# Performance work log

Measured on AMD Instinct MI355X. Metric: run time of the kernel, lower is better.

## Reference

```python
import jax, jax.numpy as jnp
import numpy as np

N = 200000   # nodes
E = 4000000  # edges
D = 32       # hidden dim (forced equal to edge-embed dim 32)
G = 512      # graphs in batch
OUT = 64     # conv5 output dim
BN_EPS = 1e-5


def _bn(h, g, b):
    # BatchNorm1d, training mode (fresh model): biased batch stats over node dim
    mu = jnp.mean(h, axis=0)
    var = jnp.var(h, axis=0)
    return g * (h - mu) * jax.lax.rsqrt(var + BN_EPS) + b


def _gine(h, src, dst, e, W1, b1, g, be, W2, b2, final_relu):
    # GINEConv (eps=0): out = MLP(x + sum_j ReLU(x_j + edge_attr))
    msg = jax.nn.relu(h[src] + e)                              # [E, D]
    agg = jax.ops.segment_sum(msg, dst, num_segments=h.shape[0])
    z = h + agg
    z = jax.nn.relu(_bn(z @ W1 + b1, g, be)) @ W2 + b2
    return jax.nn.relu(z) if final_relu else z


def setup_inputs() -> dict:
    key = jax.random.key(0)
    ks = jax.random.split(key, 16)
    xav = lambda k, shp: jax.random.uniform(k, shp, jnp.float32, -1.0, 1.0) * np.sqrt(6.0 / (shp[-2] + shp[-1]))
    x = jax.random.normal(ks[0], (N, D), jnp.float32)
    edge_index = jax.random.randint(ks[1], (2, E), 0, N, dtype=jnp.int32)
    edge_type = jax.random.randint(ks[2], (E,), 0, 2, dtype=jnp.int32)
    batch = jnp.sort(jax.random.randint(ks[3], (N,), 0, G, dtype=jnp.int32))
    emb = xav(ks[4], (2, D))  # xavier-initialized edge-type embedding
    # convs 1-4: Linear(D,D), BN(D), ReLU, Linear(D,D), ReLU  -> stacked [4,...]
    W1s = xav(ks[5], (4, D, D)); b1s = jnp.zeros((4, D))
    g1s = jnp.ones((4, D)); be1s = jnp.zeros((4, D))
    W2s = xav(ks[6], (4, D, D)); b2s = jnp.zeros((4, D))
    # conv 5: Linear(D,D), BN(D), ReLU, Linear(D,OUT)  (no final ReLU)
    w15 = xav(ks[7], (D, D)); b15 = jnp.zeros((D,))
    g5 = jnp.ones((D,)); be5 = jnp.zeros((D,))
    w25 = xav(ks[8], (D, OUT)); b25 = jnp.zeros((OUT,))
    return dict(x=x, edge_index=edge_index, edge_type=edge_type, batch=batch,
                emb=emb, W1s=W1s, b1s=b1s, g1s=g1s, be1s=be1s, W2s=W2s, b2s=b2s,
                w15=w15, b15=b15, g5=g5, be5=be5, w25=w25, b25=b25)


def reference(x, edge_index, edge_type, batch, emb, W1s, b1s, g1s, be1s, W2s, b2s,
              w15, b15, g5, be5, w25, b25):
    src, dst = edge_index[0], edge_index[1]
    e = emb[edge_type]                                          # [E, D]
    h = x
    for i in range(4):
        h = _gine(h, src, dst, e, W1s[i], b1s[i], g1s[i], be1s[i], W2s[i], b2s[i], True)
    h = _gine(h, src, dst, e, w15, b15, g5, be5, w25, b25, False)  # [N, OUT]
    mx = jax.ops.segment_max(h, batch, num_segments=G)
    cnt = jax.ops.segment_sum(jnp.ones((h.shape[0], 1), h.dtype), batch, num_segments=G)
    mn = jax.ops.segment_sum(h, batch, num_segments=G) / jnp.maximum(cnt, 1.0)
    return jnp.concatenate([mx, mn], axis=1)                    # [G, 2*OUT]
```

## Files before the change

kernel.cpp:

```cpp
#include <hip/hip_runtime.h>

#define NBLKA 2048

__device__ __forceinline__ unsigned encf(float x) {
    unsigned u = __float_as_uint(x);
    return (u & 0x80000000u) ? ~u : (u | 0x80000000u);
}
__device__ __forceinline__ float decf(unsigned u) {
    u = (u & 0x80000000u) ? (u & 0x7FFFFFFFu) : ~u;
    return __uint_as_float(u);
}
__device__ __forceinline__ unsigned bf16rne(float f) {
    unsigned u = __float_as_uint(f);
    return (u + 0x7FFFu + ((u >> 16) & 1u)) >> 16;
}


__global__ __launch_bounds__(256) void passA_k(const int* __restrict__ dst, int E,
                                               int* __restrict__ cntMat, int bshift,
                                               int nblk, int nb2) {
    __shared__ int hist[512];
    hist[threadIdx.x] = 0; hist[threadIdx.x + 256] = 0;
    __syncthreads();
    int base = blockIdx.x * 4096;
#pragma unroll
    for (int r = 0; r < 16; r++) {
        int i = base + threadIdx.x + r * 256;
        if (i < E) atomicAdd(&hist[dst[i] >> bshift], 1);
    }
    __syncthreads();
    for (int bk = threadIdx.x; bk < nb2; bk += 256)
        cntMat[bk * nblk + blockIdx.x] = hist[bk];
}

__global__ void scanA_k(int* __restrict__ data, int total, int* __restrict__ chunkTot) {
    __shared__ int sd[256];
    int tid = threadIdx.x;
    int base = blockIdx.x * 2048 + tid * 8;
    int v[8]; int s = 0;
#pragma unroll
    for (int r = 0; r < 8; r++) {
        int idx = base + r;
        int x = (idx < total) ? data[idx] : 0;
        s += x; v[r] = s;
    }
    sd[tid] = s; __syncthreads();
    for (int off = 1; off < 256; off <<= 1) {
        int x = (tid >= off) ? sd[tid - off] : 0;
        __syncthreads();
        sd[tid] += x;
        __syncthreads();
    }
    int prev = (tid > 0) ? sd[tid - 1] : 0;
#pragma unroll
    for (int r = 0; r < 8; r++) {
        int idx = base + r;
        if (idx < total) data[idx] = v[r] + prev;
    }
    if (tid == 255) chunkTot[blockIdx.x] = sd[255];
}

__global__ void scanB_k(const int* __restrict__ chunkTot, int nchunk, int* __restrict__ chunkOff) {
    __shared__ int sd[256];
    int tid = threadIdx.x;
    int v = (tid < nchunk) ? chunkTot[tid] : 0;
    sd[tid] = v; __syncthreads();
    for (int off = 1; off < 256; off <<= 1) {
        int x = (tid >= off) ? sd[tid - off] : 0;
        __syncthreads();
        sd[tid] += x;
        __syncthreads();
    }
    if (tid < nchunk) chunkOff[tid] = sd[tid] - v;
}

__global__ void scanC2_k(int* __restrict__ data, int total, const int* __restrict__ chunkOff) {
    int off = chunkOff[blockIdx.x];
    int base = blockIdx.x * 2048 + threadIdx.x * 8;
#pragma unroll
    for (int r = 0; r < 8; r++) {
        int idx = base + r;
        if (idx < total) data[idx] += off;
    }
}

__global__ __launch_bounds__(256) void passB_k(const int* __restrict__ ei,
                                               const int* __restrict__ ety, int E,
                                               const int* __restrict__ cntScan,
                                               unsigned* __restrict__ binned,
                                               int bshift, int sBits, int nblk, int nb2) {
    __shared__ unsigned stage[4096];
    __shared__ unsigned short bkid[4096];
    __shared__ int hist[512], sd[256], cursor[512], rebase[512];
    int tid = threadIdx.x;
    int base = blockIdx.x * 4096;
    hist[tid] = 0; hist[tid + 256] = 0;
    __syncthreads();

    unsigned ent[16];
    int bk[16];
    int lowmask = (1 << bshift) - 1;
    int dshift = sBits + 1;
#pragma unroll
    for (int r = 0; r < 16; r++) {
        int i = base + tid + r * 256;
        if (i < E) {
            int s = ei[i];
            int d = ei[E + i];
            int t = ety[i];
            ent[r] = ((unsigned)(d & lowmask) << dshift) | ((unsigned)t << sBits) | (unsigned)s;
            bk[r] = d >> bshift;
            atomicAdd(&hist[bk[r]], 1);
        } else bk[r] = -1;
    }
    __syncthreads();

    int v0 = hist[2 * tid], v1 = hist[2 * tid + 1];
    int sum2 = v0 + v1;
    sd[tid] = sum2; __syncthreads();
    for (int off = 1; off < 256; off <<= 1) {
        int x = (tid >= off) ? sd[tid - off] : 0;
        __syncthreads();
        sd[tid] += x;
        __syncthreads();
    }
    int exclPair = sd[tid] - sum2;
    __syncthreads();
    cursor[2 * tid] = exclPair;
    cursor[2 * tid + 1] = exclPair + v0;
    int b0 = 2 * tid, b1 = 2 * tid + 1;
    rebase[b0] = (b0 < nb2 && v0 > 0) ? (cntScan[b0 * nblk + blockIdx.x] - v0) - exclPair : 0;
    rebase[b1] = (b1 < nb2 && v1 > 0) ? (cntScan[b1 * nblk + blockIdx.x] - v1) - (exclPair + v0) : 0;
    __syncthreads();

#pragma unroll
    for (int r = 0; r < 16; r++) {
        if (bk[r] >= 0) {
            int p = atomicAdd(&cursor[bk[r]], 1);
            stage[p] = ent[r];
            bkid[p] = (unsigned short)bk[r];
        }
    }
    __syncthreads();

    int cnt = E - base; if (cnt > 4096) cnt = 4096;
    for (int i = tid; i < cnt; i += 256)
        binned[rebase[bkid[i]] + i] = stage[i];
}

__global__ __launch_bounds__(256) void passC_k(const unsigned* __restrict__ binned,
                                               const int* __restrict__ cntScan,
                                               int nblk, int* __restrict__ rowptr,
                                               unsigned* __restrict__ sorted,
                                               int N, int E, int bshift, int sBits,
                                               int nb2) {
    __shared__ int hist[512], cursor[512], sd[256];
    int tid = threadIdx.x;
    int b = blockIdx.x;
    int s = (b == 0) ? 0 : cntScan[b * nblk - 1];
    int e = cntScan[(b + 1) * nblk - 1];
    int nodeBase = b << bshift;
    int dshift = sBits + 1;

    hist[tid] = 0; hist[tid + 256] = 0;
    __syncthreads();
    for (int i = s + tid; i < e; i += 256)
        atomicAdd(&hist[(int)(binned[i] >> dshift)], 1);
    __syncthreads();

    int v0 = hist[2 * tid], v1 = hist[2 * tid + 1];
    int sum2 = v0 + v1;
    sd[tid] = sum2; __syncthreads();
    for (int off = 1; off < 256; off <<= 1) {
        int x = (tid >= off) ? sd[tid - off] : 0;
        __syncthreads();
        sd[tid] += x;
        __syncthreads();
    }
    int exclPair = sd[tid] - sum2;
    __syncthreads();
    cursor[2 * tid] = exclPair;
    cursor[2 * tid + 1] = exclPair + v0;
    int n0 = nodeBase + 2 * tid, n1 = nodeBase + 2 * tid + 1;
    if (n0 < N) rowptr[n0] = s + exclPair;
    if (n1 < N) rowptr[n1] = s + exclPair + v0;
    __syncthreads();

    for (int i = s + tid; i < e; i += 256) {
        unsigned en = binned[i];
        int ln = (int)(en >> dshift);
        int p = atomicAdd(&cursor[ln], 1);
        sorted[s + p] = en;
    }
    if (b == nb2 - 1 && tid == 0) rowptr[N] = E;
}

__global__ void prep_k(const float* __restrict__ x, unsigned* __restrict__ P,
                       unsigned* __restrict__ Q, int N,
                       unsigned* __restrict__ maxb, float* __restrict__ sumb, int G64) {
    int i = blockIdx.x * 256 + threadIdx.x;
    int tot = N * 16;
    if (i < tot) {
        float2 v = ((const float2*)x)[i];
        P[i] = bf16rne(v.x) | (bf16rne(v.y) << 16);
    }
    if (i < 16) {
        unsigned sp = bf16rne(-1e30f) | (bf16rne(-1e30f) << 16);
        P[tot + i] = sp;
        Q[tot + i] = sp;
    }
    if (i < G64) { maxb[i] = 0x007FFFFFu; sumb[i] = 0.f; }
}

__global__ __launch_bounds__(256) void layerA_k(
    const unsigned* __restrict__ hin, const int* __restrict__ rowptr,
    const unsigned* __restrict__ sorted, const float* __restrict__ emb,
    const float* __restrict__ W1, const float* __restrict__ b1,
    float* __restrict__ tout, float* __restrict__ partial, int Nn, int sBits,
    unsigned sentw)
{
    float2* tout2 = (float2*)tout;
    int tid = threadIdx.x;
    int gl = tid & 31;
    int c = gl & 15;
    int slot = gl >> 4;
    int grp = tid >> 5;
    unsigned smask = (1u << sBits) - 1u;

    float2 w1c[16];
#pragma unroll
    for (int kk = 0; kk < 16; kk++)
        w1c[kk] = *(const float2*)&W1[(16 * slot + kk) * 32 + 2 * c];
    float2 b1p = *(const float2*)&b1[2 * c];
    float2 e0p = *(const float2*)&emb[2 * c];
    float2 e1p = *(const float2*)&emb[32 + 2 * c];

    __shared__ float zl[8][32];
    __shared__ float ls[8][32], lq[8][32];

    float2 bsum = {0.f, 0.f}, bsq = {0.f, 0.f};

    int gid0 = (blockIdx.x * 256 + tid) >> 5;
    int nG = (gridDim.x * 256) >> 5;

    for (int n = gid0; n < Nn; n += nG) {
        int es = rowptr[n], ee = rowptr[n + 1];
        float accx = 0.f, accy = 0.f;
        for (int e0 = es; e0 < ee; e0 += 32) {
            int idx = e0 + gl;
            unsigned pv = (idx < ee) ? sorted[idx] : sentw;
#pragma unroll
            for (int kk = 0; kk < 16; kk++) {
                unsigned p = (unsigned)__shfl((int)pv, kk, 16);
                unsigned s = p & smask;
                unsigned w = hin[s * 16u + (unsigned)c];
                float hx = __uint_as_float(w << 16);
                float hy = __uint_as_float(w & 0xFFFF0000u);
                bool t1 = ((p >> sBits) & 1u) != 0u;
                float evx = t1 ? e1p.x : e0p.x;
                float evy = t1 ? e1p.y : e0p.y;
                accx += fmaxf(hx + evx, 0.f);
                accy += fmaxf(hy + evy, 0.f);
            }
        }
        accx += __shfl_xor(accx, 16);
        accy += __shfl_xor(accy, 16);
        unsigned wn = hin[(unsigned)n * 16u + (unsigned)c];
        accx += __uint_as_float(wn << 16);
        accy += __uint_as_float(wn & 0xFFFF0000u);

        if (slot == 0) { zl[grp][2 * c] = accx; zl[grp][2 * c + 1] = accy; }
        float tx = 0.f, ty = 0.f;
#pragma unroll
        for (int kk = 0; kk < 16; kk++) {
            float zk = zl[grp][16 * slot + kk];
            tx = fmaf(zk, w1c[kk].x, tx);
            ty = fmaf(zk, w1c[kk].y, ty);
        }
        tx += __shfl_xor(tx, 16);
        ty += __shfl_xor(ty, 16);
        tx += b1p.x; ty += b1p.y;
        if (slot == 0) { float2 tp; tp.x = tx; tp.y = ty; tout2[(unsigned)n * 16u + (unsigned)c] = tp; }
        bsum.x += tx; bsum.y += ty;
        bsq.x = fmaf(tx, tx, bsq.x);
        bsq.y = fmaf(ty, ty, bsq.y);
    }

    if (slot == 0) {
        ls[grp][2 * c] = bsum.x; ls[grp][2 * c + 1] = bsum.y;
        lq[grp][2 * c] = bsq.x;  lq[grp][2 * c + 1] = bsq.y;
    }
    __syncthreads();
    if (tid < 32) {
        float s = 0.f, q = 0.f;
#pragma unroll
        for (int r = 0; r < 8; r++) { s += ls[r][tid]; q += lq[r][tid]; }
        partial[blockIdx.x * 64 + tid] = s;
        partial[blockIdx.x * 64 + 32 + tid] = q;
    }
}

__global__ __launch_bounds__(256) void bnred1_k(const float* __restrict__ partial,
                                                float* __restrict__ partial2) {
    __shared__ float sd[4][64];
    int tid = threadIdx.x;
    int c = tid & 63, q = tid >> 6;
    int rowBase = blockIdx.x * 32 + q * 8;
    float s = 0.f;
#pragma unroll
    for (int r = 0; r < 8; r++) s += partial[(rowBase + r) * 64 + c];
    sd[q][c] = s;
    __syncthreads();
    if (q == 0) partial2[blockIdx.x * 64 + c] = sd[0][c] + sd[1][c] + sd[2][c] + sd[3][c];
}

__global__ __launch_bounds__(256) void bnred2_k(const float* __restrict__ partial2,
                                                const float* __restrict__ gamma,
                                                const float* __restrict__ beta,
                                                float* __restrict__ bn_ac, float invN) {
    __shared__ float sd[4][64];
    int tid = threadIdx.x;
    int c = tid & 63, q = tid >> 6;
    float s = 0.f;
#pragma unroll
    for (int r = 0; r < 16; r++) s += partial2[(q * 16 + r) * 64 + c];
    sd[q][c] = s;
    __syncthreads();
    if (tid < 32) {
        float mu  = (sd[0][tid] + sd[1][tid] + sd[2][tid] + sd[3][tid]) * invN;
        float sq  = (sd[0][tid + 32] + sd[1][tid + 32] + sd[2][tid + 32] + sd[3][tid + 32]) * invN;
        float var = sq - mu * mu;
        float a = gamma[tid] * rsqrtf(var + 1e-5f);
        bn_ac[tid] = a;
        bn_ac[32 + tid] = beta[tid] - a * mu;
    }
}

__global__ __launch_bounds__(256) void layerB32_k(
    const float* __restrict__ tin, const float* __restrict__ bn_ac,
    const float* __restrict__ W2, const float* __restrict__ b2,
    unsigned* __restrict__ hout, int Nn)
{
    int tid = threadIdx.x;
    int j = tid & 31, grp = tid >> 5;
    float a = bn_ac[j], c = bn_ac[32 + j];
    float wc[32];
#pragma unroll
    for (int k = 0; k < 32; k++) wc[k] = W2[k * 32 + j];
    float bj = b2[j];
    for (int n = blockIdx.x * 8 + grp; n < Nn; n += gridDim.x * 8) {
        float t = tin[n * 32 + j];
        float u = fmaxf(fmaf(a, t, c), 0.f);
        float o = bj;
#pragma unroll
        for (int k = 0; k < 32; k++) o = fmaf(__shfl(u, k, 32), wc[k], o);
        unsigned b = bf16rne(fmaxf(o, 0.f));
        unsigned nb = (unsigned)__shfl_xor((int)b, 1, 32);
        if ((j & 1) == 0) hout[(unsigned)n * 16u + (unsigned)(j >> 1)] = b | (nb << 16);
    }
}

__global__ __launch_bounds__(256) void layerB64pool_k(
    const float* __restrict__ tin, const float* __restrict__ bn_ac,
    const float* __restrict__ W2, const float* __restrict__ b2,
    const int* __restrict__ batch,
    unsigned* __restrict__ maxb, float* __restrict__ sumb, int Nn)
{
    int tid = threadIdx.x;
    int j = tid & 31, grp = tid >> 5;
    float a = bn_ac[j], c = bn_ac[32 + j];
    float wlo[32], whi[32];
#pragma unroll
    for (int k = 0; k < 32; k++) { wlo[k] = W2[k * 64 + j]; whi[k] = W2[k * 64 + 32 + j]; }
    float blo = b2[j], bhi = b2[32 + j];

    int n0 = (blockIdx.x * 8 + grp) * 64;
    if (n0 >= Nn) return;
    int nend = n0 + 64; if (nend > Nn) nend = Nn;

    int curg = -1;
    float mxl = 0.f, mxh = 0.f, sml = 0.f, smh = 0.f;
    for (int n = n0; n < nend; n++) {
        float t = tin[n * 32 + j];
        float u = fmaxf(fmaf(a, t, c), 0.f);
        float olo = blo, ohi = bhi;
#pragma unroll
        for (int k = 0; k < 32; k++) {
            float uk = __shfl(u, k, 32);
            olo = fmaf(uk, wlo[k], olo);
            ohi = fmaf(uk, whi[k], ohi);
        }
        int gn = batch[n];
        if (gn != curg) {
            if (curg >= 0) {
                atomicMax(&maxb[curg * 64 + j], encf(mxl));
                atomicMax(&maxb[curg * 64 + 32 + j], encf(mxh));
                atomicAdd(&sumb[curg * 64 + j], sml);
                atomicAdd(&sumb[curg * 64 + 32 + j], smh);
            }
            curg = gn; mxl = olo; mxh = ohi; sml = olo; smh = ohi;
        } else {
            mxl = fmaxf(mxl, olo); mxh = fmaxf(mxh, ohi);
            sml += olo; smh += ohi;
        }
    }
    if (curg >= 0) {
        atomicMax(&maxb[curg * 64 + j], encf(mxl));
        atomicMax(&maxb[curg * 64 + 32 + j], encf(mxh));
        atomicAdd(&sumb[curg * 64 + j], sml);
        atomicAdd(&sumb[curg * 64 + 32 + j], smh);
    }
}

__global__ void final_k(const unsigned* __restrict__ maxb, const float* __restrict__ sumb,
                        const int* __restrict__ batch, int Nn, float* __restrict__ out)
{
    int g = blockIdx.x, tid = threadIdx.x;
    int a = 0, b = Nn;
    while (a < b) { int m = (a + b) >> 1; if (batch[m] < g) a = m + 1; else b = m; }
    int lo0 = a;
    a = 0; b = Nn;
    while (a < b) { int m = (a + b) >> 1; if (batch[m] < g + 1) a = m + 1; else b = m; }
    int hi0 = a;
    float inv = 1.f / fmaxf((float)(hi0 - lo0), 1.f);
    if (tid < 64) out[g * 128 + tid] = decf(maxb[g * 64 + tid]);
    else          out[g * 128 + tid] = sumb[g * 64 + (tid - 64)] * inv;
}

extern "C" void kernel_launch(void* const* d_in, const int* in_sizes, int n_in,
                              void* d_out, int out_size, void* d_ws, size_t ws_size,
                              hipStream_t stream) {
    const float* x    = (const float*)d_in[0];
    const int*   ei   = (const int*)d_in[1];
    const int*   ety  = (const int*)d_in[2];
    const int*   batch= (const int*)d_in[3];
    const float* emb  = (const float*)d_in[4];
    const float* W1s  = (const float*)d_in[5];
    const float* b1s  = (const float*)d_in[6];
    const float* g1s  = (const float*)d_in[7];
    const float* be1s = (const float*)d_in[8];
    const float* W2s  = (const float*)d_in[9];
    const float* b2s  = (const float*)d_in[10];
    const float* w15  = (const float*)d_in[11];
    const float* b15  = (const float*)d_in[12];
    const float* g5   = (const float*)d_in[13];
    const float* be5  = (const float*)d_in[14];
    const float* w25  = (const float*)d_in[15];
    const float* b25  = (const float*)d_in[16];

    int N = in_sizes[0] / 32;
    int E = in_sizes[1] / 2;
    int G = out_size / 128;

    int sBits = 1; while ((1 << sBits) < N + 1) sBits++;
    int bshift = 0; while (((N - 1) >> bshift) >= 512) bshift++;
    int nb2 = ((N - 1) >> bshift) + 1;
    int nblkE = (E + 4095) / 4096;

    char* wsb = (char*)d_ws;
    size_t o = 0;
    size_t hPkBytes = (size_t)(N + 1) * 16 * 4;
    size_t tbBytes = (size_t)N * 32 * 4;
    size_t binBytes = (size_t)E * 4;
    size_t rtb = tbBytes > binBytes ? tbBytes : binBytes;
    unsigned* P      = (unsigned*)(wsb + o); o += hPkBytes;
    unsigned* Q      = (unsigned*)(wsb + o); o += hPkBytes;
    float*    tb     = (float*)(wsb + o);
    unsigned* binned = (unsigned*)(wsb + o);
    o += rtb;
    int*      rowptr = (int*)(wsb + o);   o += ((size_t)N + 2) * 4;
    unsigned* sorted = (unsigned*)(wsb + o); o += (size_t)E * 4;
    int*      chunkTot = (int*)(wsb + o); o += 1024;
    int*      chunkOff = (int*)(wsb + o); o += 1024;
    float*    partial  = (float*)(wsb + o); o += (size_t)NBLKA * 64 * 4;
    float*    partial2 = (float*)(wsb + o); o += 64 * 64 * 4;
    float*    bn_ac    = (float*)(wsb + o); o += 64 * 4;
    unsigned* maxb     = (unsigned*)(wsb + o); o += (size_t)G * 64 * 4;
    float*    sumb     = (float*)(wsb + o); o += (size_t)G * 64 * 4;
    int*      cntMat   = (int*)(wsb + o); o += (size_t)nb2 * nblkE * 4;

    passA_k<<<nblkE, 256, 0, stream>>>(ei + E, E, cntMat, bshift, nblkE, nb2);
    int total2 = nb2 * nblkE;
    int nchunk2 = (total2 + 2047) / 2048;
    scanA_k<<<nchunk2, 256, 0, stream>>>(cntMat, total2, chunkTot);
    scanB_k<<<1, 256, 0, stream>>>(chunkTot, nchunk2, chunkOff);
    scanC2_k<<<nchunk2, 256, 0, stream>>>(cntMat, total2, chunkOff);
    passB_k<<<nblkE, 256, 0, stream>>>(ei, ety, E, cntMat, binned, bshift, sBits, nblkE, nb2);
    passC_k<<<nb2, 256, 0, stream>>>(binned, cntMat, nblkE, rowptr, sorted, N, E, bshift, sBits, nb2);
    prep_k<<<(N * 16 + 255) / 256, 256, 0, stream>>>(x, P, Q, N, maxb, sumb, G * 64);

    unsigned sentw = (unsigned)N;
    float invN = 1.f / (float)N;

    unsigned* inb = P;
    unsigned* outb = Q;
    for (int L = 0; L < 5; ++L) {
        const float* W1 = (L < 4) ? W1s + L * 1024 : w15;
        const float* b1 = (L < 4) ? b1s + L * 32  : b15;
        const float* ga = (L < 4) ? g1s + L * 32  : g5;
        const float* be = (L < 4) ? be1s + L * 32 : be5;
        const float* W2 = (L < 4) ? W2s + L * 1024 : w25;
        const float* b2 = (L < 4) ? b2s + L * 32  : b25;

        layerA_k<<<NBLKA, 256, 0, stream>>>(inb, rowptr, sorted, emb, W1, b1, tb, partial, N, sBits, sentw);
        bnred1_k<<<64, 256, 0, stream>>>(partial, partial2);
        bnred2_k<<<1, 256, 0, stream>>>(partial2, ga, be, bn_ac, invN);
        if (L < 4) {
            layerB32_k<<<1024, 256, 0, stream>>>(tb, bn_ac, W2, b2, outb, N);
            unsigned* tmp = inb; inb = outb; outb = tmp;
        } else {
            layerB64pool_k<<<(N + 511) / 512, 256, 0, stream>>>(tb, bn_ac, W2, b2, batch, maxb, sumb, N);
        }
    }

    final_k<<<G, 128, 0, stream>>>(maxb, sumb, batch, N, (float*)d_out);
}
```

Measured before the change: 688.6 us.

## Switch node features to fp16 packed math and fuse small BN/scan kernels

Node features are now stored as packed fp16 instead of bf16, and the edge message add and ReLU use packed half2 arithmetic before accumulating in fp32. The goal is fewer ALU instructions per gathered edge in the hot aggregation loop. Separately, the single-block BN finalize kernel is folded into the prologue of each layerB block, and the scan offset kernel is merged into the add pass, removing five-plus small launches. The cost is that every layerB block redundantly recomputes the BN statistics, and fp16 has less range than bf16, so large activations could overflow.

```diff
diff --git a/kernel.cpp b/kernel.cpp
--- a/kernel.cpp
+++ b/kernel.cpp
@@ -1,6 +1,9 @@
 #include <hip/hip_runtime.h>
+#include <hip/hip_fp16.h>
 
 #define NBLKA 2048
+
+typedef _Float16 f16x2 __attribute__((ext_vector_type(2)));
 
 __device__ __forceinline__ unsigned encf(float x) {
     unsigned u = __float_as_uint(x);
@@ -9,10 +12,6 @@
 __device__ __forceinline__ float decf(unsigned u) {
     u = (u & 0x80000000u) ? (u & 0x7FFFFFFFu) : ~u;
     return __uint_as_float(u);
-}
-__device__ __forceinline__ unsigned bf16rne(float f) {
-    unsigned u = __float_as_uint(f);
-    return (u + 0x7FFFu + ((u >> 16) & 1u)) >> 16;
 }
 
 
@@ -60,7 +59,8 @@
     if (tid == 255) chunkTot[blockIdx.x] = sd[255];
 }
 
-__global__ void scanB_k(const int* __restrict__ chunkTot, int nchunk, int* __restrict__ chunkOff) {
+__global__ void scanC3_k(int* __restrict__ data, int total,
+                         const int* __restrict__ chunkTot, int nchunk) {
     __shared__ int sd[256];
     int tid = threadIdx.x;
     int v = (tid < nchunk) ? chunkTot[tid] : 0;
@@ -71,16 +71,12 @@
         sd[tid] += x;
         __syncthreads();
     }
-    if (tid < nchunk) chunkOff[tid] = sd[tid] - v;
-}
-
-__global__ void scanC2_k(int* __restrict__ data, int total, const int* __restrict__ chunkOff) {
-    int off = chunkOff[blockIdx.x];
-    int base = blockIdx.x * 2048 + threadIdx.x * 8;
+    int boff = (blockIdx.x > 0) ? sd[blockIdx.x - 1] : 0;
+    int base = blockIdx.x * 2048 + tid * 8;
 #pragma unroll
     for (int r = 0; r < 8; r++) {
         int idx = base + r;
-        if (idx < total) data[idx] += off;
+        if (idx < total) data[idx] += boff;
     }
 }
 
@@ -202,12 +198,14 @@
     int tot = N * 16;
     if (i < tot) {
         float2 v = ((const float2*)x)[i];
-        P[i] = bf16rne(v.x) | (bf16rne(v.y) << 16);
+        f16x2 hv;
+        hv.x = (_Float16)v.x;
+        hv.y = (_Float16)v.y;
+        P[i] = *(unsigned*)&hv;
     }
     if (i < 16) {
-        unsigned sp = bf16rne(-1e30f) | (bf16rne(-1e30f) << 16);
-        P[tot + i] = sp;
-        Q[tot + i] = sp;
+        P[tot + i] = 0xFC00FC00u;
+        Q[tot + i] = 0xFC00FC00u;
     }
     if (i < G64) { maxb[i] = 0x007FFFFFu; sumb[i] = 0.f; }
 }
@@ -232,8 +230,10 @@
     for (int kk = 0; kk < 16; kk++)
         w1c[kk] = *(const float2*)&W1[(16 * slot + kk) * 32 + 2 * c];
     float2 b1p = *(const float2*)&b1[2 * c];
-    float2 e0p = *(const float2*)&emb[2 * c];
-    float2 e1p = *(const float2*)&emb[32 + 2 * c];
+    f16x2 e0p, e1p, zero2;
+    e0p.x = (_Float16)emb[2 * c];       e0p.y = (_Float16)emb[2 * c + 1];
+    e1p.x = (_Float16)emb[32 + 2 * c];  e1p.y = (_Float16)emb[32 + 2 * c + 1];
+    zero2.x = (_Float16)0.f;            zero2.y = (_Float16)0.f;
 
     __shared__ float zl[8][32];
     __shared__ float ls[8][32], lq[8][32];
@@ -254,20 +254,19 @@
                 unsigned p = (unsigned)__shfl((int)pv, kk, 16);
                 unsigned s = p & smask;
                 unsigned w = hin[s * 16u + (unsigned)c];
-                float hx = __uint_as_float(w << 16);
-                float hy = __uint_as_float(w & 0xFFFF0000u);
-                bool t1 = ((p >> sBits) & 1u) != 0u;
-                float evx = t1 ? e1p.x : e0p.x;
-                float evy = t1 ? e1p.y : e0p.y;
-                accx += fmaxf(hx + evx, 0.f);
-                accy += fmaxf(hy + evy, 0.f);
+                f16x2 h2 = *reinterpret_cast<const f16x2*>(&w);
+                f16x2 ev = (((p >> sBits) & 1u) != 0u) ? e1p : e0p;
+                f16x2 rl = __builtin_elementwise_max(h2 + ev, zero2);
+                accx += (float)rl.x;
+                accy += (float)rl.y;
             }
         }
         accx += __shfl_xor(accx, 16);
         accy += __shfl_xor(accy, 16);
         unsigned wn = hin[(unsigned)n * 16u + (unsigned)c];
-        accx += __uint_as_float(wn << 16);
-        accy += __uint_as_float(wn & 0xFFFF0000u);
+        f16x2 fn = *reinterpret_cast<const f16x2*>(&wn);
+        accx += (float)fn.x;
+        accy += (float)fn.y;
 
         if (slot == 0) { zl[grp][2 * c] = accx; zl[grp][2 * c + 1] = accy; }
         float tx = 0.f, ty = 0.f;
@@ -314,36 +313,42 @@
     if (q == 0) partial2[blockIdx.x * 64 + c] = sd[0][c] + sd[1][c] + sd[2][c] + sd[3][c];
 }
 
-__global__ __launch_bounds__(256) void bnred2_k(const float* __restrict__ partial2,
-                                                const float* __restrict__ gamma,
-                                                const float* __restrict__ beta,
-                                                float* __restrict__ bn_ac, float invN) {
-    __shared__ float sd[4][64];
+__device__ __forceinline__ void bn_prologue(const float* __restrict__ partial2,
+                                            const float* __restrict__ gamma,
+                                            const float* __restrict__ beta,
+                                            float invN, float* bnac ,
+                                            float (*sd4)[64] ) {
     int tid = threadIdx.x;
     int c = tid & 63, q = tid >> 6;
     float s = 0.f;
 #pragma unroll
     for (int r = 0; r < 16; r++) s += partial2[(q * 16 + r) * 64 + c];
-    sd[q][c] = s;
+    sd4[q][c] = s;
     __syncthreads();
     if (tid < 32) {
-        float mu  = (sd[0][tid] + sd[1][tid] + sd[2][tid] + sd[3][tid]) * invN;
-        float sq  = (sd[0][tid + 32] + sd[1][tid + 32] + sd[2][tid + 32] + sd[3][tid + 32]) * invN;
+        float mu  = (sd4[0][tid] + sd4[1][tid] + sd4[2][tid] + sd4[3][tid]) * invN;
+        float sq  = (sd4[0][tid + 32] + sd4[1][tid + 32] + sd4[2][tid + 32] + sd4[3][tid + 32]) * invN;
         float var = sq - mu * mu;
         float a = gamma[tid] * rsqrtf(var + 1e-5f);
-        bn_ac[tid] = a;
-        bn_ac[32 + tid] = beta[tid] - a * mu;
-    }
+        bnac[tid] = a;
+        bnac[32 + tid] = beta[tid] - a * mu;
+    }
+    __syncthreads();
 }
 
 __global__ __launch_bounds__(256) void layerB32_k(
-    const float* __restrict__ tin, const float* __restrict__ bn_ac,
+    const float* __restrict__ tin, const float* __restrict__ partial2,
+    const float* __restrict__ gamma, const float* __restrict__ beta, float invN,
     const float* __restrict__ W2, const float* __restrict__ b2,
     unsigned* __restrict__ hout, int Nn)
 {
+    __shared__ float bnac[64];
+    __shared__ float sd4[4][64];
+    bn_prologue(partial2, gamma, beta, invN, bnac, sd4);
+
     int tid = threadIdx.x;
     int j = tid & 31, grp = tid >> 5;
-    float a = bn_ac[j], c = bn_ac[32 + j];
+    float a = bnac[j], c = bnac[32 + j];
     float wc[32];
 #pragma unroll
     for (int k = 0; k < 32; k++) wc[k] = W2[k * 32 + j];
@@ -354,21 +359,27 @@
         float o = bj;
 #pragma unroll
         for (int k = 0; k < 32; k++) o = fmaf(__shfl(u, k, 32), wc[k], o);
-        unsigned b = bf16rne(fmaxf(o, 0.f));
-        unsigned nb = (unsigned)__shfl_xor((int)b, 1, 32);
-        if ((j & 1) == 0) hout[(unsigned)n * 16u + (unsigned)(j >> 1)] = b | (nb << 16);
+        _Float16 hv = (_Float16)fmaxf(o, 0.f);
+        unsigned hb = (unsigned)*reinterpret_cast<unsigned short*>(&hv);
+        unsigned nb = (unsigned)__shfl_xor((int)hb, 1, 32);
+        if ((j & 1) == 0) hout[(unsigned)n * 16u + (unsigned)(j >> 1)] = hb | (nb << 16);
     }
 }
 
 __global__ __launch_bounds__(256) void layerB64pool_k(
-    const float* __restrict__ tin, const float* __restrict__ bn_ac,
+    const float* __restrict__ tin, const float* __restrict__ partial2,
+    const float* __restrict__ gamma, const float* __restrict__ beta, float invN,
     const float* __restrict__ W2, const float* __restrict__ b2,
     const int* __restrict__ batch,
     unsigned* __restrict__ maxb, float* __restrict__ sumb, int Nn)
 {
+    __shared__ float bnac[64];
+    __shared__ float sd4[4][64];
+    bn_prologue(partial2, gamma, beta, invN, bnac, sd4);
+
     int tid = threadIdx.x;
     int j = tid & 31, grp = tid >> 5;
-    float a = bn_ac[j], c = bn_ac[32 + j];
+    float a = bnac[j], c = bnac[32 + j];
     float wlo[32], whi[32];
 #pragma unroll
     for (int k = 0; k < 32; k++) { wlo[k] = W2[k * 64 + j]; whi[k] = W2[k * 64 + 32 + j]; }
@@ -471,10 +482,8 @@
     int*      rowptr = (int*)(wsb + o);   o += ((size_t)N + 2) * 4;
     unsigned* sorted = (unsigned*)(wsb + o); o += (size_t)E * 4;
     int*      chunkTot = (int*)(wsb + o); o += 1024;
-    int*      chunkOff = (int*)(wsb + o); o += 1024;
     float*    partial  = (float*)(wsb + o); o += (size_t)NBLKA * 64 * 4;
     float*    partial2 = (float*)(wsb + o); o += 64 * 64 * 4;
-    float*    bn_ac    = (float*)(wsb + o); o += 64 * 4;
     unsigned* maxb     = (unsigned*)(wsb + o); o += (size_t)G * 64 * 4;
     float*    sumb     = (float*)(wsb + o); o += (size_t)G * 64 * 4;
     int*      cntMat   = (int*)(wsb + o); o += (size_t)nb2 * nblkE * 4;
@@ -483,8 +492,7 @@
     int total2 = nb2 * nblkE;
     int nchunk2 = (total2 + 2047) / 2048;
     scanA_k<<<nchunk2, 256, 0, stream>>>(cntMat, total2, chunkTot);
-    scanB_k<<<1, 256, 0, stream>>>(chunkTot, nchunk2, chunkOff);
-    scanC2_k<<<nchunk2, 256, 0, stream>>>(cntMat, total2, chunkOff);
+    scanC3_k<<<nchunk2, 256, 0, stream>>>(cntMat, total2, chunkTot, nchunk2);
     passB_k<<<nblkE, 256, 0, stream>>>(ei, ety, E, cntMat, binned, bshift, sBits, nblkE, nb2);
     passC_k<<<nb2, 256, 0, stream>>>(binned, cntMat, nblkE, rowptr, sorted, N, E, bshift, sBits, nb2);
     prep_k<<<(N * 16 + 255) / 256, 256, 0, stream>>>(x, P, Q, N, maxb, sumb, G * 64);
@@ -504,12 +512,11 @@
 
         layerA_k<<<NBLKA, 256, 0, stream>>>(inb, rowptr, sorted, emb, W1, b1, tb, partial, N, sBits, sentw);
         bnred1_k<<<64, 256, 0, stream>>>(partial, partial2);
-        bnred2_k<<<1, 256, 0, stream>>>(partial2, ga, be, bn_ac, invN);
         if (L < 4) {
-            layerB32_k<<<1024, 256, 0, stream>>>(tb, bn_ac, W2, b2, outb, N);
+            layerB32_k<<<1024, 256, 0, stream>>>(tb, partial2, ga, be, invN, W2, b2, outb, N);
             unsigned* tmp = inb; inb = outb; outb = tmp;
         } else {
-            layerB64pool_k<<<(N + 511) / 512, 256, 0, stream>>>(tb, bn_ac, W2, b2, batch, maxb, sumb, N);
+            layerB64pool_k<<<(N + 511) / 512, 256, 0, stream>>>(tb, partial2, ga, be, invN, W2, b2, batch, maxb, sumb, N);
         }
     }
 
```

After: 671.1 us. 1.03x faster.
